# Kernel tuning notes

Measured on AMD Instinct MI355X. Metric: run time of the kernel, lower is better.

Reference implementation:

```python
import jax, jax.numpy as jnp
import numpy as np


def setup_inputs() -> dict:
    key = jax.random.key(0)
    k1, k2, k3 = jax.random.split(key, 3)
    B, H, W, A, NC, C = 16, 38, 38, 4, 21, 64
    return {
        "cls_pred": jax.random.normal(k1, (B, H, W, A * NC), dtype=jnp.float32),
        "source": jax.random.normal(k2, (B, C, H, W), dtype=jnp.float32),
        "cls_r_prob": jax.random.uniform(k3, (NC, NC), dtype=jnp.float32),
        "num_classes": NC,
    }


def reference(cls_pred, source, cls_r_prob, num_classes):
    B = cls_pred.shape[0]
    L = cls_pred.shape[1] * cls_pred.shape[2]  # H*W spatial locations (38*38=1444)

    # softmax over classes, then regroup anchors per spatial location
    scores = jax.nn.softmax(cls_pred.reshape(B, -1, num_classes), axis=-1)
    regional = scores.reshape(B, L, -1)                     # [B, L, A*num_classes]
    cls_idx = jnp.argmax(regional, axis=-1) % num_classes   # [B, L] int

    # build_local_graph (vectorized): lower triangle from pairwise class lookup,
    # symmetrize, add identity only where class != 0 (background)
    P = cls_r_prob[cls_idx[:, :, None], cls_idx[:, None, :]]  # [B, L, L] gather
    lower = jnp.tril(P, k=-1)
    G = lower + jnp.swapaxes(lower, 1, 2)
    diag = (cls_idx != 0).astype(P.dtype)                    # [B, L]
    G = G + jnp.eye(L, dtype=P.dtype)[None] * diag[:, :, None]

    # source: NCHW -> [B, L, C], then graph aggregation via batched matmul
    src = jnp.transpose(source, (0, 2, 3, 1)).reshape(B, L, -1)
    fused = jnp.einsum('bij,bjc->bic', G, src)               # [B, L, C]
    return (fused, src)
```

## Files before the change

### kernel.cpp

```cpp
#include <hip/hip_runtime.h>
#include <math.h>

#define Bn 16
#define Ln 1444
#define NCn 21
#define Cn 64
#define NBn 23
#define KC 1344

__global__ __launch_bounds__(256) void kB(const float* __restrict__ cls_pred,
                                          const float* __restrict__ source,
                                          const float* __restrict__ R,
                                          int* __restrict__ cls_idx,
                                          float* __restrict__ src_out,
                                          float* __restrict__ bs,
                                          float2* __restrict__ Gg) {
    int b = blockIdx.x & 15, m = blockIdx.x >> 4;
    int base = m * 64;
    int lane = threadIdx.x & 63, grp = threadIdx.x >> 6;
    __shared__ float sh[9536];
    __shared__ int cls[64];
    float (*tile)[65] = (float(*)[65])sh;
    float* clsP = sh + 4160;
    float* WS   = sh + 4160;

    if (blockIdx.x == 0) {
        for (int i = threadIdx.x; i < 441; i += 256) {
            int a = i / 21, k = i % 21;
            float rak = R[a * 21 + k], rka = R[k * 21 + a];
            Gg[i] = make_float2(rak - rka, rka);
        }
    }

#pragma unroll
    for (int cc = 0; cc < 16; cc++) {
        int c = grp * 16 + cc;
        float v = 0.f;
        if (base + lane < Ln) v = source[((size_t)b * Cn + c) * Ln + base + lane];
        tile[c][lane] = v;
    }
    {
        const float4* gp = reinterpret_cast<const float4*>(cls_pred + ((size_t)b * Ln + base) * 84);
        int lim4 = (Ln - base) * 21;
#pragma unroll
        for (int it = 0; it < 6; it++) {
            int f4 = threadIdx.x + it * 256;
            if (f4 < 1344) {
                float4 v = (f4 < lim4) ? gp[f4] : make_float4(0.f, 0.f, 0.f, 0.f);
                reinterpret_cast<float4*>(clsP)[f4] = v;
            }
        }
    }
    __syncthreads();

    {
        int p = threadIdx.x >> 2, a = threadIdx.x & 3;
        bool valid = (base + p < Ln);
        const float* q = clsP + p * 84 + a * 21;
        float x[21];
#pragma unroll
        for (int i = 0; i < 21; i++) x[i] = q[i];
        float mx = x[0];
#pragma unroll
        for (int i = 1; i < 21; i++) mx = fmaxf(mx, x[i]);
        float s = 0.f;
#pragma unroll
        for (int i = 0; i < 21; i++) { x[i] = expf(x[i] - mx); s += x[i]; }
        float best = -1.f; int bi = 0;
#pragma unroll
        for (int i = 0; i < 21; i++) {
            float sm = x[i] / s;
            if (sm > best) { best = sm; bi = a * 21 + i; }
        }
#pragma unroll
        for (int d = 1; d <= 2; d <<= 1) {
            float ob = __shfl_xor(best, d);
            int oi = __shfl_xor(bi, d);
            if (ob > best || (ob == best && oi < bi)) { best = ob; bi = oi; }
        }
        if (a == 0) {
            if (valid) { int k = bi % 21; cls[p] = k; cls_idx[b * Ln + base + p] = k; }
            else cls[p] = 255;
        }
    }
    __syncthreads();

    float cs[21];
#pragma unroll
    for (int k = 0; k < 21; k++) cs[k] = 0.f;
#pragma unroll
    for (int jj = 0; jj < 16; jj++) {
        int j = grp * 16 + jj;
        float v = tile[lane][j];
        if (base + j < Ln) src_out[((size_t)b * Ln + base + j) * Cn + lane] = v;
        int k = cls[j];
#pragma unroll
        for (int kk = 0; kk < 21; kk++) cs[kk] += (kk == k) ? v : 0.f;
    }
#pragma unroll
    for (int kk = 0; kk < 21; kk++) WS[grp * KC + kk * 64 + lane] = cs[kk];
    __syncthreads();

    for (int i = threadIdx.x; i < KC; i += 256) {
        float v = WS[i] + WS[KC + i] + WS[2 * KC + i] + WS[3 * KC + i];
        bs[((size_t)b * NBn + m) * KC + i] = v;
    }
}

__global__ __launch_bounds__(512, 2) void kC(const float* __restrict__ src,
                                             const int* __restrict__ cls_idx,
                                             const float2* __restrict__ Gg,
                                             const float* __restrict__ bs,
                                             float* __restrict__ fused) {
    int b = blockIdx.x & 15, m = blockIdx.x >> 4;
    int base = m * 64;
    int lane = threadIdx.x & 63, grp = threadIdx.x >> 6;
    __shared__ float PS[KC];
    __shared__ float Tt[KC];
    __shared__ float WS[8][KC];
    __shared__ int cls[64];

    float sT[8];
#pragma unroll
    for (int t = 0; t < 8; t++) {
        int i = grp * 8 + t;
        sT[t] = (base + i < Ln) ? src[((size_t)b * Ln + base + i) * Cn + lane] : 0.f;
    }
    if (threadIdx.x < 64) {
        int k = 0;
        if (base + (int)threadIdx.x < Ln) k = cls_idx[b * Ln + base + threadIdx.x];
        cls[threadIdx.x] = k;
    }
    if (threadIdx.x < KC / 4) {
        int g = threadIdx.x;
        float rx = 0.f, ry = 0.f, rz = 0.f, rw = 0.f;
        float px = 0.f, py = 0.f, pz = 0.f, pw = 0.f;
#pragma unroll
        for (int mm = 0; mm < NBn; mm++) {
            float4 v = *reinterpret_cast<const float4*>(&bs[((size_t)b * NBn + mm) * KC + g * 4]);
            rx += v.x; ry += v.y; rz += v.z; rw += v.w;
            if (mm < m) { px += v.x; py += v.y; pz += v.z; pw += v.w; }
        }
        PS[g * 4] = px; PS[g * 4 + 1] = py; PS[g * 4 + 2] = pz; PS[g * 4 + 3] = pw;
        Tt[g * 4] = rx; Tt[g * 4 + 1] = ry; Tt[g * 4 + 2] = rz; Tt[g * 4 + 3] = rw;
    }
    __syncthreads();

    int cj[8];
#pragma unroll
    for (int j = 0; j < 8; j++) cj[j] = cls[grp * 8 + j];

    {
        float cs[21];
#pragma unroll
        for (int k = 0; k < 21; k++) cs[k] = 0.f;
#pragma unroll
        for (int t = 0; t < 8; t++) {
            int k = cj[t];
#pragma unroll
            for (int kk = 0; kk < 21; kk++) cs[kk] += (kk == k) ? sT[t] : 0.f;
        }
#pragma unroll
        for (int kk = 0; kk < 21; kk++) WS[grp][kk * 64 + lane] = cs[kk];
    }
    __syncthreads();

    for (int i = threadIdx.x; i < KC; i += 512) {
        float run = PS[i];
#pragma unroll
        for (int g = 0; g < 8; g++) {
            float w = WS[g][i];
            WS[g][i] = run;
            run += w;
        }
    }
    __syncthreads();

    float Tc[21], msW[21];
#pragma unroll
    for (int k = 0; k < 21; k++) Tc[k] = Tt[k * 64 + lane];
#pragma unroll
    for (int k = 0; k < 21; k++) msW[k] = WS[grp][k * 64 + lane];

    int nvalid = (Ln - base < 64) ? (Ln - base) : 64;
#pragma unroll
    for (int t = 0; t < 8; t++) {
        int i = grp * 8 + t;
        if (i < nvalid) {
            int cis = __builtin_amdgcn_readfirstlane(cj[t]);
            const float2* grow = Gg + cis * 21;
            float sv = sT[t];
            float accA = (((cis != 0) ? 1.f : 0.f) - grow[cis].y) * sv;
            float accB = 0.f;
#pragma unroll
            for (int k = 0; k < 21; k++) {
                float2 w = grow[k];
                accA = fmaf(w.x, msW[k], accA);
                accB = fmaf(w.y, Tc[k], accB);
            }
#pragma unroll
            for (int j = 0; j < 8; j++)
                if (j < t) {
                    int cjs = __builtin_amdgcn_readfirstlane(cj[j]);
                    accA = fmaf(grow[cjs].x, sT[j], accA);
                }
            fused[((size_t)b * Ln + base + i) * Cn + lane] = accA + accB;
        }
    }
}

extern "C" void kernel_launch(void* const* d_in, const int* in_sizes, int n_in,
                              void* d_out, int out_size, void* d_ws, size_t ws_size,
                              hipStream_t stream) {
    const float* cls_pred = (const float*)d_in[0];
    const float* source = (const float*)d_in[1];
    const float* cls_r_prob = (const float*)d_in[2];

    float* fused = (float*)d_out;
    float* src_out = fused + (size_t)Bn * Ln * Cn;

    char* w = (char*)d_ws;
    int* cls_idx = (int*)w;
    size_t off = ((size_t)Bn * Ln * 4 + 1023) & ~(size_t)1023;
    float* bs = (float*)(w + off);
    float2* Gg = (float2*)(w + off + (size_t)Bn * NBn * KC * 4);

    hipLaunchKernelGGL(kB, dim3(Bn * NBn), dim3(256), 0, stream,
                       cls_pred, source, cls_r_prob, cls_idx, src_out, bs, Gg);
    hipLaunchKernelGGL(kC, dim3(Bn * NBn), dim3(512), 0, stream,
                       src_out, cls_idx, Gg, bs, fused);
}
```

Measured before the change: 29.17 us.

## Move intra-block graph aggregation into first kernel, add per-class cross-block correction

The first kernel now runs with 512 threads and computes the within-block part of the graph aggregation directly: it builds per-warp class sums with a local exclusive prefix scan and writes a partial fused output, reading the class-relation matrix straight from global memory instead of a precomputed pair table. The second kernel no longer reloads source features or redoes the per-row work. It builds a 21x64 per-class correction from the cross-block prefix sums and totals, then adds that to fused with a read-modify-write. This cuts redundant loads and compute in the second kernel, at the cost of extra global traffic on fused and uncached R lookups in the inner loop.

```diff
diff --git a/kernel.cpp b/kernel.cpp
--- a/kernel.cpp
+++ b/kernel.cpp
@@ -7,34 +7,26 @@
 #define Cn 64
 #define NBn 23
 #define KC 1344
-
-__global__ __launch_bounds__(256) void kB(const float* __restrict__ cls_pred,
-                                          const float* __restrict__ source,
-                                          const float* __restrict__ R,
-                                          int* __restrict__ cls_idx,
-                                          float* __restrict__ src_out,
-                                          float* __restrict__ bs,
-                                          float2* __restrict__ Gg) {
+#define NG 336
+
+__global__ __launch_bounds__(512, 2) void kB(const float* __restrict__ cls_pred,
+                                             const float* __restrict__ source,
+                                             const float* __restrict__ R,
+                                             int* __restrict__ cls_idx,
+                                             float* __restrict__ src_out,
+                                             float* __restrict__ bs,
+                                             float* __restrict__ fused) {
     int b = blockIdx.x & 15, m = blockIdx.x >> 4;
     int base = m * 64;
     int lane = threadIdx.x & 63, grp = threadIdx.x >> 6;
-    __shared__ float sh[9536];
+    __shared__ float tile[64][65];
+    __shared__ float WSb[8 * KC];
     __shared__ int cls[64];
-    float (*tile)[65] = (float(*)[65])sh;
-    float* clsP = sh + 4160;
-    float* WS   = sh + 4160;
-
-    if (blockIdx.x == 0) {
-        for (int i = threadIdx.x; i < 441; i += 256) {
-            int a = i / 21, k = i % 21;
-            float rak = R[a * 21 + k], rka = R[k * 21 + a];
-            Gg[i] = make_float2(rak - rka, rka);
-        }
-    }
-
-#pragma unroll
-    for (int cc = 0; cc < 16; cc++) {
-        int c = grp * 16 + cc;
+    float* clsP = WSb;
+
+#pragma unroll
+    for (int cc = 0; cc < 8; cc++) {
+        int c = grp * 8 + cc;
         float v = 0.f;
         if (base + lane < Ln) v = source[((size_t)b * Cn + c) * Ln + base + lane];
         tile[c][lane] = v;
@@ -43,8 +35,8 @@
         const float4* gp = reinterpret_cast<const float4*>(cls_pred + ((size_t)b * Ln + base) * 84);
         int lim4 = (Ln - base) * 21;
 #pragma unroll
-        for (int it = 0; it < 6; it++) {
-            int f4 = threadIdx.x + it * 256;
+        for (int it = 0; it < 3; it++) {
+            int f4 = threadIdx.x + it * 512;
             if (f4 < 1344) {
                 float4 v = (f4 < lim4) ? gp[f4] : make_float4(0.f, 0.f, 0.f, 0.f);
                 reinterpret_cast<float4*>(clsP)[f4] = v;
@@ -53,7 +45,7 @@
     }
     __syncthreads();
 
-    {
+    if (threadIdx.x < 256) {
         int p = threadIdx.x >> 2, a = threadIdx.x & 3;
         bool valid = (base + p < Ln);
         const float* q = clsP + p * 84 + a * 21;
@@ -82,129 +74,128 @@
             if (valid) { int k = bi % 21; cls[p] = k; cls_idx[b * Ln + base + p] = k; }
             else cls[p] = 255;
         }
-    }
-    __syncthreads();
-
-    float cs[21];
-#pragma unroll
-    for (int k = 0; k < 21; k++) cs[k] = 0.f;
-#pragma unroll
-    for (int jj = 0; jj < 16; jj++) {
-        int j = grp * 16 + jj;
-        float v = tile[lane][j];
-        if (base + j < Ln) src_out[((size_t)b * Ln + base + j) * Cn + lane] = v;
-        int k = cls[j];
-#pragma unroll
-        for (int kk = 0; kk < 21; kk++) cs[kk] += (kk == k) ? v : 0.f;
-    }
-#pragma unroll
-    for (int kk = 0; kk < 21; kk++) WS[grp * KC + kk * 64 + lane] = cs[kk];
-    __syncthreads();
-
-    for (int i = threadIdx.x; i < KC; i += 256) {
-        float v = WS[i] + WS[KC + i] + WS[2 * KC + i] + WS[3 * KC + i];
-        bs[((size_t)b * NBn + m) * KC + i] = v;
+    } else {
+        int g2 = grp - 4;
+#pragma unroll
+        for (int jj = 0; jj < 16; jj++) {
+            int j = g2 * 16 + jj;
+            if (base + j < Ln) src_out[((size_t)b * Ln + base + j) * Cn + lane] = tile[lane][j];
+        }
+    }
+    __syncthreads();
+
+    int cj[8]; float sT[8];
+#pragma unroll
+    for (int t = 0; t < 8; t++) {
+        cj[t] = cls[grp * 8 + t];
+        sT[t] = tile[lane][grp * 8 + t];
+    }
+    {
+        float cs[21];
+#pragma unroll
+        for (int k = 0; k < 21; k++) cs[k] = 0.f;
+#pragma unroll
+        for (int t = 0; t < 8; t++) {
+            int k = cj[t];
+#pragma unroll
+            for (int kk = 0; kk < 21; kk++) cs[kk] += (kk == k) ? sT[t] : 0.f;
+        }
+#pragma unroll
+        for (int kk = 0; kk < 21; kk++) WSb[grp * KC + kk * 64 + lane] = cs[kk];
+    }
+    __syncthreads();
+
+    for (int i = threadIdx.x; i < KC; i += 512) {
+        float run = 0.f;
+#pragma unroll
+        for (int g = 0; g < 8; g++) {
+            float w = WSb[g * KC + i];
+            WSb[g * KC + i] = run;
+            run += w;
+        }
+        bs[((size_t)b * NBn + m) * KC + i] = run;
+    }
+    __syncthreads();
+
+    float msW[21];
+#pragma unroll
+    for (int k = 0; k < 21; k++) msW[k] = WSb[grp * KC + k * 64 + lane];
+    int nvalid = (Ln - base < 64) ? (Ln - base) : 64;
+#pragma unroll
+    for (int t = 0; t < 8; t++) {
+        int i = grp * 8 + t;
+        if (i < nvalid) {
+            int cis = __builtin_amdgcn_readfirstlane(cj[t]);
+            const float* rrow = R + cis * 21;
+            float sv = sT[t];
+            float acc = (((cis != 0) ? 1.f : 0.f) - rrow[cis]) * sv;
+#pragma unroll
+            for (int k = 0; k < 21; k++)
+                acc = fmaf(rrow[k] - R[k * 21 + cis], msW[k], acc);
+#pragma unroll
+            for (int j = 0; j < 8; j++)
+                if (j < t) {
+                    int cjs = __builtin_amdgcn_readfirstlane(cj[j]);
+                    acc = fmaf(rrow[cjs] - R[cjs * 21 + cis], sT[j], acc);
+                }
+            fused[((size_t)b * Ln + base + i) * Cn + lane] = acc;
+        }
     }
 }
 
-__global__ __launch_bounds__(512, 2) void kC(const float* __restrict__ src,
-                                             const int* __restrict__ cls_idx,
-                                             const float2* __restrict__ Gg,
-                                             const float* __restrict__ bs,
-                                             float* __restrict__ fused) {
+__global__ __launch_bounds__(512) void kC(const int* __restrict__ cls_idx,
+                                          const float* __restrict__ R,
+                                          const float* __restrict__ bs,
+                                          float* __restrict__ fused) {
     int b = blockIdx.x & 15, m = blockIdx.x >> 4;
     int base = m * 64;
     int lane = threadIdx.x & 63, grp = threadIdx.x >> 6;
     __shared__ float PS[KC];
     __shared__ float Tt[KC];
-    __shared__ float WS[8][KC];
+    __shared__ float U[KC];
     __shared__ int cls[64];
 
-    float sT[8];
-#pragma unroll
-    for (int t = 0; t < 8; t++) {
-        int i = grp * 8 + t;
-        sT[t] = (base + i < Ln) ? src[((size_t)b * Ln + base + i) * Cn + lane] : 0.f;
+    if (threadIdx.x < NG) {
+        int g = threadIdx.x;
+        float rx = 0.f, ry = 0.f, rz = 0.f, rw = 0.f;
+        float px = 0.f, py = 0.f, pz = 0.f, pw = 0.f;
+#pragma unroll
+        for (int mm = 0; mm < NBn; mm++) {
+            float4 v = *reinterpret_cast<const float4*>(&bs[((size_t)b * NBn + mm) * KC + g * 4]);
+            rx += v.x; ry += v.y; rz += v.z; rw += v.w;
+            if (mm < m) { px += v.x; py += v.y; pz += v.z; pw += v.w; }
+        }
+        PS[g * 4] = px; PS[g * 4 + 1] = py; PS[g * 4 + 2] = pz; PS[g * 4 + 3] = pw;
+        Tt[g * 4] = rx; Tt[g * 4 + 1] = ry; Tt[g * 4 + 2] = rz; Tt[g * 4 + 3] = rw;
     }
     if (threadIdx.x < 64) {
         int k = 0;
         if (base + (int)threadIdx.x < Ln) k = cls_idx[b * Ln + base + threadIdx.x];
         cls[threadIdx.x] = k;
     }
-    if (threadIdx.x < KC / 4) {
-        int g = threadIdx.x;
-        float rx = 0.f, ry = 0.f, rz = 0.f, rw = 0.f;
-        float px = 0.f, py = 0.f, pz = 0.f, pw = 0.f;
-#pragma unroll
-        for (int mm = 0; mm < NBn; mm++) {
-            float4 v = *reinterpret_cast<const float4*>(&bs[((size_t)b * NBn + mm) * KC + g * 4]);
-            rx += v.x; ry += v.y; rz += v.z; rw += v.w;
-            if (mm < m) { px += v.x; py += v.y; pz += v.z; pw += v.w; }
-        }
-        PS[g * 4] = px; PS[g * 4 + 1] = py; PS[g * 4 + 2] = pz; PS[g * 4 + 3] = pw;
-        Tt[g * 4] = rx; Tt[g * 4 + 1] = ry; Tt[g * 4 + 2] = rz; Tt[g * 4 + 3] = rw;
-    }
-    __syncthreads();
-
-    int cj[8];
-#pragma unroll
-    for (int j = 0; j < 8; j++) cj[j] = cls[grp * 8 + j];
-
-    {
-        float cs[21];
-#pragma unroll
-        for (int k = 0; k < 21; k++) cs[k] = 0.f;
-#pragma unroll
-        for (int t = 0; t < 8; t++) {
-            int k = cj[t];
-#pragma unroll
-            for (int kk = 0; kk < 21; kk++) cs[kk] += (kk == k) ? sT[t] : 0.f;
-        }
-#pragma unroll
-        for (int kk = 0; kk < 21; kk++) WS[grp][kk * 64 + lane] = cs[kk];
-    }
-    __syncthreads();
-
-    for (int i = threadIdx.x; i < KC; i += 512) {
-        float run = PS[i];
-#pragma unroll
-        for (int g = 0; g < 8; g++) {
-            float w = WS[g][i];
-            WS[g][i] = run;
-            run += w;
-        }
-    }
-    __syncthreads();
-
-    float Tc[21], msW[21];
-#pragma unroll
-    for (int k = 0; k < 21; k++) Tc[k] = Tt[k * 64 + lane];
-#pragma unroll
-    for (int k = 0; k < 21; k++) msW[k] = WS[grp][k * 64 + lane];
+    __syncthreads();
+
+    for (int a = grp; a < 21; a += 8) {
+        const float* rrow = R + a * 21;
+        float acc = 0.f;
+#pragma unroll
+        for (int k = 0; k < 21; k++) {
+            float rak = rrow[k], rka = R[k * 21 + a];
+            acc = fmaf(rak - rka, PS[k * 64 + lane], acc);
+            acc = fmaf(rka, Tt[k * 64 + lane], acc);
+        }
+        U[a * 64 + lane] = acc;
+    }
+    __syncthreads();
 
     int nvalid = (Ln - base < 64) ? (Ln - base) : 64;
 #pragma unroll
     for (int t = 0; t < 8; t++) {
         int i = grp * 8 + t;
         if (i < nvalid) {
-            int cis = __builtin_amdgcn_readfirstlane(cj[t]);
-            const float2* grow = Gg + cis * 21;
-            float sv = sT[t];
-            float accA = (((cis != 0) ? 1.f : 0.f) - grow[cis].y) * sv;
-            float accB = 0.f;
-#pragma unroll
-            for (int k = 0; k < 21; k++) {
-                float2 w = grow[k];
-                accA = fmaf(w.x, msW[k], accA);
-                accB = fmaf(w.y, Tc[k], accB);
-            }
-#pragma unroll
-            for (int j = 0; j < 8; j++)
-                if (j < t) {
-                    int cjs = __builtin_amdgcn_readfirstlane(cj[j]);
-                    accA = fmaf(grow[cjs].x, sT[j], accA);
-                }
-            fused[((size_t)b * Ln + base + i) * Cn + lane] = accA + accB;
+            int ci = cls[i];
+            size_t o = ((size_t)b * Ln + base + i) * Cn + lane;
+            fused[o] += U[ci * 64 + lane];
         }
     }
 }
@@ -223,10 +214,9 @@
     int* cls_idx = (int*)w;
     size_t off = ((size_t)Bn * Ln * 4 + 1023) & ~(size_t)1023;
     float* bs = (float*)(w + off);
-    float2* Gg = (float2*)(w + off + (size_t)Bn * NBn * KC * 4);
-
-    hipLaunchKernelGGL(kB, dim3(Bn * NBn), dim3(256), 0, stream,
-                       cls_pred, source, cls_r_prob, cls_idx, src_out, bs, Gg);
+
+    hipLaunchKernelGGL(kB, dim3(Bn * NBn), dim3(512), 0, stream,
+                       cls_pred, source, cls_r_prob, cls_idx, src_out, bs, fused);
     hipLaunchKernelGGL(kC, dim3(Bn * NBn), dim3(512), 0, stream,
-                       src_out, cls_idx, Gg, bs, fused);
+                       cls_idx, cls_r_prob, bs, fused);
 }
```

Result: slower. 31.65 us (+8.5%).

## Process two 64-row tiles per block to share the block-sum prefix reduction

Applied to the files above, without the earlier changes.

Both kernels now handle a pair of adjacent 64-location tiles per block, with a doubled thread count and per-half shared-memory buffers. The grid shrinks from 23 to 12 blocks per batch. In kC, one pass over the per-tile class sums builds the prefix sums for both tiles and the shared total, which halves redundant reads of the bs workspace. The cost is fewer, larger blocks (192 total), which may leave some CUs idle. The padded 24th tile is guarded out.

```diff
diff --git a/kernel.cpp b/kernel.cpp
--- a/kernel.cpp
+++ b/kernel.cpp
@@ -6,32 +6,35 @@
 #define NCn 21
 #define Cn 64
 #define NBn 23
+#define NPAIR 12
 #define KC 1344
 
-__global__ __launch_bounds__(256) void kB(const float* __restrict__ cls_pred,
+__global__ __launch_bounds__(512) void kB(const float* __restrict__ cls_pred,
                                           const float* __restrict__ source,
                                           const float* __restrict__ R,
                                           int* __restrict__ cls_idx,
                                           float* __restrict__ src_out,
                                           float* __restrict__ bs,
                                           float2* __restrict__ Gg) {
-    int b = blockIdx.x & 15, m = blockIdx.x >> 4;
+    int b = blockIdx.x & 15, q = blockIdx.x >> 4;
+    int half = threadIdx.x >> 8;
+    int tid = threadIdx.x & 255;
+    int m = 2 * q + half;
     int base = m * 64;
-    int lane = threadIdx.x & 63, grp = threadIdx.x >> 6;
-    __shared__ float sh[9536];
-    __shared__ int cls[64];
-    float (*tile)[65] = (float(*)[65])sh;
-    float* clsP = sh + 4160;
-    float* WS   = sh + 4160;
+    int lane = tid & 63, grp = tid >> 6;
+    __shared__ float sh[2][9536];
+    __shared__ int cls[2][64];
+    float (*tile)[65] = (float(*)[65])sh[half];
+    float* clsP = sh[half] + 4160;
+    float* WS   = sh[half] + 4160;
 
     if (blockIdx.x == 0) {
-        for (int i = threadIdx.x; i < 441; i += 256) {
+        for (int i = threadIdx.x; i < 441; i += 512) {
             int a = i / 21, k = i % 21;
             float rak = R[a * 21 + k], rka = R[k * 21 + a];
             Gg[i] = make_float2(rak - rka, rka);
         }
     }
-
 #pragma unroll
     for (int cc = 0; cc < 16; cc++) {
         int c = grp * 16 + cc;
@@ -44,7 +47,7 @@
         int lim4 = (Ln - base) * 21;
 #pragma unroll
         for (int it = 0; it < 6; it++) {
-            int f4 = threadIdx.x + it * 256;
+            int f4 = tid + it * 256;
             if (f4 < 1344) {
                 float4 v = (f4 < lim4) ? gp[f4] : make_float4(0.f, 0.f, 0.f, 0.f);
                 reinterpret_cast<float4*>(clsP)[f4] = v;
@@ -54,12 +57,12 @@
     __syncthreads();
 
     {
-        int p = threadIdx.x >> 2, a = threadIdx.x & 3;
+        int p = tid >> 2, a = tid & 3;
         bool valid = (base + p < Ln);
-        const float* q = clsP + p * 84 + a * 21;
+        const float* qq = clsP + p * 84 + a * 21;
         float x[21];
 #pragma unroll
-        for (int i = 0; i < 21; i++) x[i] = q[i];
+        for (int i = 0; i < 21; i++) x[i] = qq[i];
         float mx = x[0];
 #pragma unroll
         for (int i = 1; i < 21; i++) mx = fmaxf(mx, x[i]);
@@ -79,8 +82,8 @@
             if (ob > best || (ob == best && oi < bi)) { best = ob; bi = oi; }
         }
         if (a == 0) {
-            if (valid) { int k = bi % 21; cls[p] = k; cls_idx[b * Ln + base + p] = k; }
-            else cls[p] = 255;
+            if (valid) { int k = bi % 21; cls[half][p] = k; cls_idx[b * Ln + base + p] = k; }
+            else cls[half][p] = 255;
         }
     }
     __syncthreads();
@@ -93,7 +96,7 @@
         int j = grp * 16 + jj;
         float v = tile[lane][j];
         if (base + j < Ln) src_out[((size_t)b * Ln + base + j) * Cn + lane] = v;
-        int k = cls[j];
+        int k = cls[half][j];
 #pragma unroll
         for (int kk = 0; kk < 21; kk++) cs[kk] += (kk == k) ? v : 0.f;
     }
@@ -101,24 +104,29 @@
     for (int kk = 0; kk < 21; kk++) WS[grp * KC + kk * 64 + lane] = cs[kk];
     __syncthreads();
 
-    for (int i = threadIdx.x; i < KC; i += 256) {
-        float v = WS[i] + WS[KC + i] + WS[2 * KC + i] + WS[3 * KC + i];
-        bs[((size_t)b * NBn + m) * KC + i] = v;
+    if (m < NBn) {
+        for (int i = tid; i < KC; i += 256) {
+            float v = WS[i] + WS[KC + i] + WS[2 * KC + i] + WS[3 * KC + i];
+            bs[((size_t)b * NBn + m) * KC + i] = v;
+        }
     }
 }
 
-__global__ __launch_bounds__(512, 2) void kC(const float* __restrict__ src,
-                                             const int* __restrict__ cls_idx,
-                                             const float2* __restrict__ Gg,
-                                             const float* __restrict__ bs,
-                                             float* __restrict__ fused) {
-    int b = blockIdx.x & 15, m = blockIdx.x >> 4;
+__global__ __launch_bounds__(1024) void kC(const float* __restrict__ src,
+                                           const int* __restrict__ cls_idx,
+                                           const float2* __restrict__ Gg,
+                                           const float* __restrict__ bs,
+                                           float* __restrict__ fused) {
+    int b = blockIdx.x & 15, q = blockIdx.x >> 4;
+    int half = threadIdx.x >> 9;
+    int tid = threadIdx.x & 511;
+    int m = 2 * q + half;
     int base = m * 64;
-    int lane = threadIdx.x & 63, grp = threadIdx.x >> 6;
-    __shared__ float PS[KC];
+    int lane = tid & 63, grp = tid >> 6;
+    __shared__ float PS[2][KC];
     __shared__ float Tt[KC];
-    __shared__ float WS[8][KC];
-    __shared__ int cls[64];
+    __shared__ float WS[2][8][KC];
+    __shared__ int cls[2][64];
 
     float sT[8];
 #pragma unroll
@@ -126,29 +134,35 @@
         int i = grp * 8 + t;
         sT[t] = (base + i < Ln) ? src[((size_t)b * Ln + base + i) * Cn + lane] : 0.f;
     }
-    if (threadIdx.x < 64) {
+    if (threadIdx.x < 128) {
+        int h = threadIdx.x >> 6, p = threadIdx.x & 63;
+        int mm = 2 * q + h;
         int k = 0;
-        if (base + (int)threadIdx.x < Ln) k = cls_idx[b * Ln + base + threadIdx.x];
-        cls[threadIdx.x] = k;
+        if (mm * 64 + p < Ln) k = cls_idx[b * Ln + mm * 64 + p];
+        cls[h][p] = k;
     }
     if (threadIdx.x < KC / 4) {
         int g = threadIdx.x;
         float rx = 0.f, ry = 0.f, rz = 0.f, rw = 0.f;
-        float px = 0.f, py = 0.f, pz = 0.f, pw = 0.f;
+        float ax = 0.f, ay = 0.f, az = 0.f, aw = 0.f;
+        float bx = 0.f, by = 0.f, bz = 0.f, bw = 0.f;
+        int mA = 2 * q, mB = 2 * q + 1;
 #pragma unroll
         for (int mm = 0; mm < NBn; mm++) {
             float4 v = *reinterpret_cast<const float4*>(&bs[((size_t)b * NBn + mm) * KC + g * 4]);
             rx += v.x; ry += v.y; rz += v.z; rw += v.w;
-            if (mm < m) { px += v.x; py += v.y; pz += v.z; pw += v.w; }
-        }
-        PS[g * 4] = px; PS[g * 4 + 1] = py; PS[g * 4 + 2] = pz; PS[g * 4 + 3] = pw;
+            if (mm < mA) { ax += v.x; ay += v.y; az += v.z; aw += v.w; }
+            if (mm < mB) { bx += v.x; by += v.y; bz += v.z; bw += v.w; }
+        }
+        PS[0][g * 4] = ax; PS[0][g * 4 + 1] = ay; PS[0][g * 4 + 2] = az; PS[0][g * 4 + 3] = aw;
+        PS[1][g * 4] = bx; PS[1][g * 4 + 1] = by; PS[1][g * 4 + 2] = bz; PS[1][g * 4 + 3] = bw;
         Tt[g * 4] = rx; Tt[g * 4 + 1] = ry; Tt[g * 4 + 2] = rz; Tt[g * 4 + 3] = rw;
     }
     __syncthreads();
 
     int cj[8];
 #pragma unroll
-    for (int j = 0; j < 8; j++) cj[j] = cls[grp * 8 + j];
+    for (int j = 0; j < 8; j++) cj[j] = cls[half][grp * 8 + j];
 
     {
         float cs[21];
@@ -161,16 +175,18 @@
             for (int kk = 0; kk < 21; kk++) cs[kk] += (kk == k) ? sT[t] : 0.f;
         }
 #pragma unroll
-        for (int kk = 0; kk < 21; kk++) WS[grp][kk * 64 + lane] = cs[kk];
-    }
-    __syncthreads();
-
-    for (int i = threadIdx.x; i < KC; i += 512) {
-        float run = PS[i];
+        for (int kk = 0; kk < 21; kk++) WS[half][grp][kk * 64 + lane] = cs[kk];
+    }
+    __syncthreads();
+
+    for (int i = threadIdx.x; i < 2 * KC; i += 1024) {
+        int h = (i >= KC) ? 1 : 0;
+        int j = i - h * KC;
+        float run = PS[h][j];
 #pragma unroll
         for (int g = 0; g < 8; g++) {
-            float w = WS[g][i];
-            WS[g][i] = run;
+            float w = WS[h][g][j];
+            WS[h][g][j] = run;
             run += w;
         }
     }
@@ -180,9 +196,10 @@
 #pragma unroll
     for (int k = 0; k < 21; k++) Tc[k] = Tt[k * 64 + lane];
 #pragma unroll
-    for (int k = 0; k < 21; k++) msW[k] = WS[grp][k * 64 + lane];
-
-    int nvalid = (Ln - base < 64) ? (Ln - base) : 64;
+    for (int k = 0; k < 21; k++) msW[k] = WS[half][grp][k * 64 + lane];
+
+    int nvalid = Ln - base;
+    if (nvalid > 64) nvalid = 64;
 #pragma unroll
     for (int t = 0; t < 8; t++) {
         int i = grp * 8 + t;
@@ -225,8 +242,8 @@
     float* bs = (float*)(w + off);
     float2* Gg = (float2*)(w + off + (size_t)Bn * NBn * KC * 4);
 
-    hipLaunchKernelGGL(kB, dim3(Bn * NBn), dim3(256), 0, stream,
+    hipLaunchKernelGGL(kB, dim3(Bn * NPAIR), dim3(512), 0, stream,
                        cls_pred, source, cls_r_prob, cls_idx, src_out, bs, Gg);
-    hipLaunchKernelGGL(kC, dim3(Bn * NBn), dim3(512), 0, stream,
+    hipLaunchKernelGGL(kC, dim3(Bn * NPAIR), dim3(1024), 0, stream,
                        src_out, cls_idx, Gg, bs, fused);
 }
```

Result: slower. 30.39 us (+4.2%).
